# Kernel optimization log

Measured on AMD Instinct MI355X. Metric: run time of the kernel, lower is better.

The kernel has to match this reference:

```python
import jax, jax.numpy as jnp
import numpy as np

K = 3   # 4D kernel size
P = 1   # padding (all 4 dims)
S = 1   # stride (all 4 dims)
DIL = 1 # dilation

def setup_inputs() -> dict:
    key = jax.random.key(0)
    k1, k2, k3 = jax.random.split(key, 3)
    x = jax.random.normal(k1, (2, 8, 16, 40, 40, 40), dtype=jnp.float32)
    # K separate Conv3d layers: weight[i] has shape [C_o, C_i, K, K, K]
    weight = jax.random.normal(k2, (K, 32, 8, K, K, K), dtype=jnp.float32) * 0.05
    bias = jax.random.normal(k3, (K, 32), dtype=jnp.float32) * 0.05
    return {"x": x, "weight": weight, "bias": bias}

def reference(x, weight, bias):
    # x: [B, C_i, T, D, H, W]; weight: [K, C_o, C_i, K, K, K]; bias: [K, C_o]
    B, Ci, T, D, H, W = x.shape
    Co = weight.shape[1]
    O = (T + 2 * P - K) // S + 1
    # Fold temporal frames into the batch dim and all K conv3d filters into
    # the output-channel dim -> a single conv3d replaces K*T launches.
    x2 = jnp.transpose(x, (0, 2, 1, 3, 4, 5)).reshape(B * T, Ci, D, H, W)
    w = weight.reshape(K * Co, Ci, K, K, K)
    y = jax.lax.conv_general_dilated(
        x2, w,
        window_strides=(S, S, S),
        padding=[(P, P)] * 3,
        rhs_dilation=(DIL, DIL, DIL),
        dimension_numbers=("NCDHW", "OIDHW", "NCDHW"),
    )  # [B*T, K*Co, Dp, Hp, Wp]
    Dp, Hp, Wp = y.shape[-3:]
    y = y.reshape(B, T, K, Co, Dp, Hp, Wp)
    # bias is added per Conv3d call, i.e. once per contributing (i, j) pair
    y = y + bias[None, None, :, :, None, None, None]
    # Temporal accumulation: out[o] = sum_i y[j = o*S + i - P, i] (skip OOB j),
    # implemented via zero-padding (padded frames contribute nothing, incl. bias).
    y_pad = jnp.pad(y, ((0, 0), (P, P), (0, 0), (0, 0), (0, 0), (0, 0), (0, 0)))
    idx = jnp.arange(O)[:, None] * S + jnp.arange(K)[None, :]  # [O, K] indices into padded T
    gathered = y_pad[:, idx, jnp.arange(K)[None, :]]  # [B, O, K, Co, Dp, Hp, Wp]
    out = gathered.sum(axis=2)  # [B, O, Co, Dp, Hp, Wp]
    return jnp.transpose(out, (0, 2, 1, 3, 4, 5))  # [B, Co, O, Dp, Hp, Wp]
```

## Files before the change

### kernel.cpp

```cpp
#include <hip/hip_runtime.h>


typedef unsigned int u32;
typedef unsigned short u16;
typedef __attribute__((ext_vector_type(8))) short short8;
typedef __attribute__((ext_vector_type(4))) float f32x4;

#define XT_OFF_BYTES 65536

__device__ __forceinline__ u32 bf16r(float f) {
    u32 u = __float_as_uint(f);
    return (u + 0x7FFFu + ((u >> 16) & 1u)) >> 16;
}

__device__ __forceinline__ void glds16(const void* g, void* l) {
    __builtin_amdgcn_global_load_lds((const __attribute__((address_space(1))) u32*)g,
                                     (__attribute__((address_space(3))) u32*)l, 16, 0, 0);
}

__global__ __launch_bounds__(256) void prep_x(const float* __restrict__ x, u16* __restrict__ xtp) {
    const int c = blockIdx.x * 256 + threadIdx.x;
    int wp = c % 42;
    int tmp = c / 42;
    const int hp = tmp % 42; tmp /= 42;
    const int dp = tmp % 42; tmp /= 42;
    const int t  = tmp % 16;
    const int b  = tmp / 16;
    const int wa = wp - 1, ha = hp - 1, da = dp - 1;
    u32 q0 = 0, q1 = 0, q2 = 0, q3 = 0;
    if ((unsigned)wa < 40u && (unsigned)ha < 40u && (unsigned)da < 40u) {
        const float* xp = x + ((b * 8) * 16 + t) * 64000 + da * 1600 + ha * 40 + wa;
        float v0 = xp[0];
        float v1 = xp[1024000];
        float v2 = xp[2048000];
        float v3 = xp[3072000];
        float v4 = xp[4096000];
        float v5 = xp[5120000];
        float v6 = xp[6144000];
        float v7 = xp[7168000];
        q0 = bf16r(v0) | (bf16r(v1) << 16);
        q1 = bf16r(v2) | (bf16r(v3) << 16);
        q2 = bf16r(v4) | (bf16r(v5) << 16);
        q3 = bf16r(v6) | (bf16r(v7) << 16);
    }
    uint4 q; q.x = q0; q.y = q1; q.z = q2; q.w = q3;
    *(uint4*)(xtp + (size_t)c * 8) = q;
}

__global__ __launch_bounds__(256) void prep_w(const float* __restrict__ wgt, u16* __restrict__ wf) {
    const int idx = blockIdx.x * 256 + threadIdx.x;
    const int kt = idx / 7168;
    const int r  = idx - kt * 7168;
    const int s2 = r >> 9;
    const int l  = (r >> 3) & 63;
    const int j  = r & 7;
    const int co = (s2 & 1) * 16 + (l & 15);
    const int k  = (s2 >> 1) * 32 + (l >> 4) * 8 + j;
    u32 v = 0;
    if (k < 216) {
        const int ci = k & 7;
        const int combo = k >> 3;
        const int kd = combo / 9;
        const int r9 = combo - kd * 9;
        const int kh = r9 / 3;
        const int kw = r9 - kh * 3;
        v = bf16r(wgt[((kt * 32 + co) * 8 + ci) * 27 + kd * 9 + kh * 3 + kw]);
    }
    wf[idx] = (u16)v;
}

__global__ __launch_bounds__(256, 4) void conv4d_mfma(
    const u16* __restrict__ xtp, const u16* __restrict__ wf,
    const float* __restrict__ bias, float* __restrict__ out)
{
    __shared__ __align__(16) u16 sHalo[10080];
    __shared__ float sBsum[32];

    const int tid  = threadIdx.x;
    const int lane = tid & 63;
    const int wid  = tid >> 6;
    const int bi   = blockIdx.x;
    const int h0   = (bi % 5) * 8;
    const int d    = (bi / 5) % 40;
    const int o    = (bi / 200) % 16;
    const int b    = bi / 3200;

    if (tid < 32) {
        float s = 0.f;
        for (int kt = 0; kt < 3; ++kt) {
            int t = o + kt - 1;
            if ((unsigned)t < 16u) s += bias[kt * 32 + tid];
        }
        sBsum[tid] = s;
    }

    const int quad = lane >> 4;
    const int nl   = lane & 15;

    int lb[5];
#pragma unroll
    for (int tl = 0; tl < 5; ++tl) {
        int n = wid * 80 + tl * 16 + nl;
        int hh = n / 40;
        int ww = n - hh * 40;
        lb[tl] = (hh * 42 + ww) * 16;
    }

    int offs7[7];
#pragma unroll
    for (int s = 0; s < 7; ++s) {
        const int c0 = 4 * s;
        int O0 = (c0+0 < 27) ? (((c0+0)/9)*420 + (((c0+0)%9)/3)*42 + ((c0+0)%3)) * 16 : 0;
        int O1 = (c0+1 < 27) ? (((c0+1)/9)*420 + (((c0+1)%9)/3)*42 + ((c0+1)%3)) * 16 : 0;
        int O2 = (c0+2 < 27) ? (((c0+2)/9)*420 + (((c0+2)%9)/3)*42 + ((c0+2)%3)) * 16 : 0;
        int O3 = (c0+3 < 27) ? (((c0+3)/9)*420 + (((c0+3)%9)/3)*42 + ((c0+3)%3)) * 16 : 0;
        offs7[s] = (quad & 2) ? ((quad & 1) ? O3 : O2) : ((quad & 1) ? O1 : O0);
    }

    const f32x4 zero = {0.f, 0.f, 0.f, 0.f};
    f32x4 acc[2][5];
#pragma unroll
    for (int mt = 0; mt < 2; ++mt)
#pragma unroll
        for (int tl = 0; tl < 5; ++tl) acc[mt][tl] = zero;

#pragma unroll
    for (int kt = 0; kt < 3; ++kt) {
        const int t = o + kt - 1;

        __syncthreads();
        if ((unsigned)t >= 16u) continue;

        {
            const u16* gbase = xtp + (size_t)(b * 16 + t) * 592704 + h0 * 336;
            const int jw = wid * 315;
#pragma unroll
            for (int i = 0; i < 5; ++i) {
                const int j = jw + i * 64 + lane;
                if (i < 4 || lane < 59) {
                    const int dpp = j / 420;
                    const int r = j - dpp * 420;
                    glds16(gbase + (d + dpp) * 14112 + r * 8, (char*)sHalo + (jw + i * 64) * 16);
                }
            }
        }
        __syncthreads();

        const u16* wfk = wf + kt * 7168;
#pragma unroll
        for (int s = 0; s < 7; ++s) {
            const short8 a0 = *(const short8*)(wfk + s * 1024 + lane * 8);
            const short8 a1 = *(const short8*)(wfk + s * 1024 + 512 + lane * 8);
            const int off = offs7[s];
#pragma unroll
            for (int tl = 0; tl < 5; ++tl) {
                const short8 bf = *(const short8*)((const char*)sHalo + lb[tl] + off);
                acc[0][tl] = __builtin_amdgcn_mfma_f32_16x16x32_bf16(a0, bf, acc[0][tl], 0, 0, 0);
                acc[1][tl] = __builtin_amdgcn_mfma_f32_16x16x32_bf16(a1, bf, acc[1][tl], 0, 0, 0);
            }
        }
    }

    const int coB = quad * 4;
    float bs[2][4];
#pragma unroll
    for (int mt = 0; mt < 2; ++mt)
#pragma unroll
        for (int reg = 0; reg < 4; ++reg) bs[mt][reg] = sBsum[mt * 16 + coB + reg];

#pragma unroll
    for (int mt = 0; mt < 2; ++mt)
#pragma unroll
        for (int tl = 0; tl < 5; ++tl) {
            int n = wid * 80 + tl * 16 + nl;
            int hh = n / 40;
            int ww = n - hh * 40;
            const size_t base = (size_t)(((b * 32 + mt * 16 + coB) * 16 + o)) * 64000
                              + d * 1600 + (h0 + hh) * 40 + ww;
#pragma unroll
            for (int reg = 0; reg < 4; ++reg)
                out[base + (size_t)reg * 1024000] = acc[mt][tl][reg] + bs[mt][reg];
        }
}

extern "C" void kernel_launch(void* const* d_in, const int* in_sizes, int n_in,
                              void* d_out, int out_size, void* d_ws, size_t ws_size,
                              hipStream_t stream)
{
    const float* x    = (const float*)d_in[0];
    const float* wgt  = (const float*)d_in[1];
    const float* bias = (const float*)d_in[2];
    float* out = (float*)d_out;
    u16* wfbuf = (u16*)d_ws;
    u16* xtp   = (u16*)((char*)d_ws + XT_OFF_BYTES);
    (void)in_sizes; (void)n_in; (void)out_size; (void)ws_size;

    prep_w<<<dim3(84),   dim3(256), 0, stream>>>(wgt, wfbuf);
    prep_x<<<dim3(9261), dim3(256), 0, stream>>>(x, xtp);
    conv4d_mfma<<<dim3(6400), dim3(256), 0, stream>>>(xtp, wfbuf, bias, out);
}
```

Measured before the change: 366.4 us.

## Double-buffer halo loads across temporal taps and merge prep kernels

The conv kernel now keeps two LDS halo buffers and issues the global-to-LDS load for the next temporal tap while running the MFMA compute on the current one. Out-of-range taps at the temporal edges are skipped up front rather than tested inside the loop. The occupancy hint drops from 4 to 3 blocks per SM because LDS use doubles. The weight and input prep kernels are also merged into one launch to save a kernel launch. The risks are lower occupancy and the need for the asynchronous LDS writes to be complete when each sync is reached.

```diff
diff --git a/kernel.cpp b/kernel.cpp
--- a/kernel.cpp
+++ b/kernel.cpp
@@ -18,7 +18,32 @@
                                      (__attribute__((address_space(3))) u32*)l, 16, 0, 0);
 }
 
-__global__ __launch_bounds__(256) void prep_x(const float* __restrict__ x, u16* __restrict__ xtp) {
+__global__ __launch_bounds__(256) void prep_xw(const float* __restrict__ x,
+                                               const float* __restrict__ wgt,
+                                               u16* __restrict__ xtp,
+                                               u16* __restrict__ wf) {
+    if (blockIdx.x >= 9261) {
+        const int idx = (blockIdx.x - 9261) * 256 + threadIdx.x;
+        const int kt = idx / 7168;
+        const int r  = idx - kt * 7168;
+        const int s2 = r >> 9;
+        const int l  = (r >> 3) & 63;
+        const int j  = r & 7;
+        const int co = (s2 & 1) * 16 + (l & 15);
+        const int k  = (s2 >> 1) * 32 + (l >> 4) * 8 + j;
+        u32 v = 0;
+        if (k < 216) {
+            const int ci = k & 7;
+            const int combo = k >> 3;
+            const int kd = combo / 9;
+            const int r9 = combo - kd * 9;
+            const int kh = r9 / 3;
+            const int kw = r9 - kh * 3;
+            v = bf16r(wgt[((kt * 32 + co) * 8 + ci) * 27 + kd * 9 + kh * 3 + kw]);
+        }
+        wf[idx] = (u16)v;
+        return;
+    }
     const int c = blockIdx.x * 256 + threadIdx.x;
     int wp = c % 42;
     int tmp = c / 42;
@@ -47,33 +72,11 @@
     *(uint4*)(xtp + (size_t)c * 8) = q;
 }
 
-__global__ __launch_bounds__(256) void prep_w(const float* __restrict__ wgt, u16* __restrict__ wf) {
-    const int idx = blockIdx.x * 256 + threadIdx.x;
-    const int kt = idx / 7168;
-    const int r  = idx - kt * 7168;
-    const int s2 = r >> 9;
-    const int l  = (r >> 3) & 63;
-    const int j  = r & 7;
-    const int co = (s2 & 1) * 16 + (l & 15);
-    const int k  = (s2 >> 1) * 32 + (l >> 4) * 8 + j;
-    u32 v = 0;
-    if (k < 216) {
-        const int ci = k & 7;
-        const int combo = k >> 3;
-        const int kd = combo / 9;
-        const int r9 = combo - kd * 9;
-        const int kh = r9 / 3;
-        const int kw = r9 - kh * 3;
-        v = bf16r(wgt[((kt * 32 + co) * 8 + ci) * 27 + kd * 9 + kh * 3 + kw]);
-    }
-    wf[idx] = (u16)v;
-}
-
-__global__ __launch_bounds__(256, 4) void conv4d_mfma(
+__global__ __launch_bounds__(256, 3) void conv4d_mfma(
     const u16* __restrict__ xtp, const u16* __restrict__ wf,
     const float* __restrict__ bias, float* __restrict__ out)
 {
-    __shared__ __align__(16) u16 sHalo[10080];
+    __shared__ __align__(16) u16 sHalo[2][10080];
     __shared__ float sBsum[32];
 
     const int tid  = threadIdx.x;
@@ -124,41 +127,58 @@
 #pragma unroll
         for (int tl = 0; tl < 5; ++tl) acc[mt][tl] = zero;
 
-#pragma unroll
-    for (int kt = 0; kt < 3; ++kt) {
-        const int t = o + kt - 1;
-
+    const int kt_lo = (o == 0)  ? 1 : 0;
+    const int kt_hi = (o == 15) ? 1 : 2;
+    const int nkt   = kt_hi - kt_lo + 1;
+
+#define STAGE(KT, DST)                                                                   \
+    {                                                                                    \
+        const int t_ = o + (KT) - 1;                                                     \
+        const u16* gbase_ = xtp + (size_t)(b * 16 + t_) * 592704 + h0 * 336;             \
+        const int jw_ = wid * 315;                                                       \
+        _Pragma("unroll")                                                                \
+        for (int i_ = 0; i_ < 5; ++i_) {                                                 \
+            const int j_ = jw_ + i_ * 64 + lane;                                         \
+            if (i_ < 4 || lane < 59) {                                                   \
+                const int dpp_ = j_ / 420;                                               \
+                const int r_ = j_ - dpp_ * 420;                                          \
+                glds16(gbase_ + (d + dpp_) * 14112 + r_ * 8,                             \
+                       (char*)(DST) + (jw_ + i_ * 64) * 16);                             \
+            }                                                                            \
+        }                                                                                \
+    }
+
+#define COMPUTE(KT, BUF)                                                                 \
+    {                                                                                    \
+        const u16* wfk_ = wf + (KT) * 7168;                                              \
+        _Pragma("unroll")                                                                \
+        for (int s_ = 0; s_ < 7; ++s_) {                                                 \
+            const short8 a0_ = *(const short8*)(wfk_ + s_ * 1024 + lane * 8);            \
+            const short8 a1_ = *(const short8*)(wfk_ + s_ * 1024 + 512 + lane * 8);      \
+            const int off_ = offs7[s_];                                                  \
+            _Pragma("unroll")                                                            \
+            for (int tl_ = 0; tl_ < 5; ++tl_) {                                          \
+                const short8 bf_ = *(const short8*)((const char*)(BUF) + lb[tl_] + off_);\
+                acc[0][tl_] = __builtin_amdgcn_mfma_f32_16x16x32_bf16(a0_, bf_, acc[0][tl_], 0, 0, 0); \
+                acc[1][tl_] = __builtin_amdgcn_mfma_f32_16x16x32_bf16(a1_, bf_, acc[1][tl_], 0, 0, 0); \
+            }                                                                            \
+        }                                                                                \
+    }
+
+    STAGE(kt_lo, sHalo[0]);
+    __syncthreads();
+
+    STAGE(kt_lo + 1, sHalo[1]);
+    COMPUTE(kt_lo, sHalo[0]);
+    __syncthreads();
+
+    if (nkt == 3) {
+        STAGE(kt_lo + 2, sHalo[0]);
+        COMPUTE(kt_lo + 1, sHalo[1]);
         __syncthreads();
-        if ((unsigned)t >= 16u) continue;
-
-        {
-            const u16* gbase = xtp + (size_t)(b * 16 + t) * 592704 + h0 * 336;
-            const int jw = wid * 315;
-#pragma unroll
-            for (int i = 0; i < 5; ++i) {
-                const int j = jw + i * 64 + lane;
-                if (i < 4 || lane < 59) {
-                    const int dpp = j / 420;
-                    const int r = j - dpp * 420;
-                    glds16(gbase + (d + dpp) * 14112 + r * 8, (char*)sHalo + (jw + i * 64) * 16);
-                }
-            }
-        }
-        __syncthreads();
-
-        const u16* wfk = wf + kt * 7168;
-#pragma unroll
-        for (int s = 0; s < 7; ++s) {
-            const short8 a0 = *(const short8*)(wfk + s * 1024 + lane * 8);
-            const short8 a1 = *(const short8*)(wfk + s * 1024 + 512 + lane * 8);
-            const int off = offs7[s];
-#pragma unroll
-            for (int tl = 0; tl < 5; ++tl) {
-                const short8 bf = *(const short8*)((const char*)sHalo + lb[tl] + off);
-                acc[0][tl] = __builtin_amdgcn_mfma_f32_16x16x32_bf16(a0, bf, acc[0][tl], 0, 0, 0);
-                acc[1][tl] = __builtin_amdgcn_mfma_f32_16x16x32_bf16(a1, bf, acc[1][tl], 0, 0, 0);
-            }
-        }
+        COMPUTE(kt_lo + 2, sHalo[0]);
+    } else {
+        COMPUTE(kt_lo + 1, sHalo[1]);
     }
 
     const int coB = quad * 4;
@@ -195,7 +215,6 @@
     u16* xtp   = (u16*)((char*)d_ws + XT_OFF_BYTES);
     (void)in_sizes; (void)n_in; (void)out_size; (void)ws_size;
 
-    prep_w<<<dim3(84),   dim3(256), 0, stream>>>(wgt, wfbuf);
-    prep_x<<<dim3(9261), dim3(256), 0, stream>>>(x, xtp);
+    prep_xw<<<dim3(9345), dim3(256), 0, stream>>>(x, wgt, xtp, wfbuf);
     conv4d_mfma<<<dim3(6400), dim3(256), 0, stream>>>(xtp, wfbuf, bias, out);
 }
```

New measurement: 371.3 us. Within noise of the previous version (+1.3%).
